# Kernel optimization log

Measured on AMD Instinct MI355X. Metric: run time of the kernel, lower is better.

Reference implementation:

```python
import jax, jax.numpy as jnp
import numpy as np
from math import log, sqrt

B, S, D, H, L = 16, 512, 512, 8, 6
DPH = D // H
DFF = 2048
VOCAB = 1024
MAXDEG = 64
NPC, NS = 4096, 4096


def setup_inputs() -> dict:
    rng = np.random.default_rng(0)
    raw_x = rng.integers(0, VOCAB + 1, (B, S)).astype(np.int32)
    scatter_degree = rng.integers(0, MAXDEG + 1, (B, S)).astype(np.int32)

    def uniq_triples(n, seed):
        r = np.random.default_rng(seed)
        flat = r.choice(B * S * S, n, replace=False)  # unique (b,i,j)
        b, i, j = np.unravel_index(flat, (B, S, S))
        return np.stack([b, i, j], 1).astype(np.int32)

    parentchild_indices = uniq_triples(NPC, 1)
    silbing_indices = uniq_triples(NS, 2)
    parent_child_now = np.stack([np.arange(B), rng.integers(0, S, B)], 1).astype(np.int32)
    silbing_now = np.stack([np.arange(B), rng.integers(0, S, B)], 1).astype(np.int32)

    key = jax.random.key(0)
    ks = jax.random.split(key, 16)
    sc = 0.02
    inp = {
        "raw_x": jnp.asarray(raw_x),
        "scatter_degree": jnp.asarray(scatter_degree),
        "parentchild_indices": jnp.asarray(parentchild_indices),
        "parent_child_now": jnp.asarray(parent_child_now),
        "silbing_indices": jnp.asarray(silbing_indices),
        "silbing_now": jnp.asarray(silbing_now),
        "vocab_emb": jax.random.normal(ks[0], (VOCAB + 1, D), jnp.float32) * sc,
        "degree_emb": jax.random.normal(ks[1], (MAXDEG + 1, D), jnp.float32) * sc,
        "active_rel_emb": jax.random.normal(ks[2], (2, D), jnp.float32) * sc,
        "relation_encoder": jax.random.uniform(ks[3], (3,), jnp.float32),
        "Wq": jax.random.normal(ks[4], (L, D, D), jnp.float32) * sc,
        "bq": jnp.zeros((L, D), jnp.float32),
        "Wk": jax.random.normal(ks[5], (L, D, D), jnp.float32) * sc,
        "bk": jnp.zeros((L, D), jnp.float32),
        "Wv": jax.random.normal(ks[6], (L, D, D), jnp.float32) * sc,
        "bv": jnp.zeros((L, D), jnp.float32),
        "Wo": jax.random.normal(ks[7], (L, D, D), jnp.float32) * sc,
        "bo": jnp.zeros((L, D), jnp.float32),
        "W1": jax.random.normal(ks[8], (L, DFF, D), jnp.float32) * sc,
        "b1": jnp.zeros((L, DFF), jnp.float32),
        "W2": jax.random.normal(ks[9], (L, D, DFF), jnp.float32) * sc,
        "b2": jnp.zeros((L, D), jnp.float32),
        "ln_g": jnp.ones((L, D), jnp.float32),
        "ln_b": jnp.zeros((L, D), jnp.float32),
        "logits_w": jax.random.normal(ks[10], (VOCAB, D), jnp.float32) * sc,
    }
    return inp


def _layer_norm(x, g, b):
    m = jnp.mean(x, -1, keepdims=True)
    v = jnp.mean((x - m) ** 2, -1, keepdims=True)  # biased var, eps=1e-5 (torch default)
    return (x - m) * jax.lax.rsqrt(v + 1e-5) * g + b


def _forward(raw_x, scatter_degree, parentchild_indices, parent_child_now,
             silbing_indices, silbing_now, vocab_emb, degree_emb, active_rel_emb,
             relation_encoder, Wq, bq, Wk, bk, Wv, bv, Wo, bo, W1, b1, W2, b2,
             ln_g, ln_b, logits_w):
    x = vocab_emb[raw_x]  # [B,S,D]
    # sinusoidal positional encoding
    pos = jnp.arange(S, dtype=jnp.float32)[:, None]
    div = jnp.exp(jnp.arange(0, D, 2, dtype=jnp.float32) * (-log(10000.0) / D))
    pe = jnp.zeros((S, D), x.dtype).at[:, 0::2].set(jnp.sin(pos * div)).at[:, 1::2].set(jnp.cos(pos * div))
    x = x + pe
    # structural encodings
    x = x + degree_emb[scatter_degree]
    x = x.at[parent_child_now[:, 0], parent_child_now[:, 1]].add(active_rel_emb[0])
    x = x.at[silbing_now[:, 0], silbing_now[:, 1]].add(active_rel_emb[1])

    pb, pi, pj = parentchild_indices[:, 0], parentchild_indices[:, 1], parentchild_indices[:, 2]
    sb, si, sj = silbing_indices[:, 0], silbing_indices[:, 1], silbing_indices[:, 2]
    inv_norm = 1.0 / sqrt(DPH)

    for l in range(L):
        q = (x @ Wq[l].T + bq[l]).reshape(B, S, H, DPH).transpose(0, 2, 1, 3)
        k = (x @ Wk[l].T + bk[l]).reshape(B, S, H, DPH).transpose(0, 2, 1, 3)
        v = (x @ Wv[l].T + bv[l]).reshape(B, S, H, DPH).transpose(0, 2, 1, 3)
        scores = jnp.einsum('bhqd,bhkd->bhqk', q, k) * inv_norm  # [B,H,S,S]
        # scatter-added relational bias (broadcast over all heads)
        scores = scores.at[pb, :, pi, pj].add(relation_encoder[0])
        scores = scores.at[pb, :, pj, pi].add(relation_encoder[1])
        scores = scores.at[sb, :, si, sj].add(relation_encoder[2])
        scores = scores.at[sb, :, sj, si].add(relation_encoder[2])
        attn = jax.nn.softmax(scores, axis=-1)
        o = jnp.einsum('bhqk,bhkd->bhqd', attn, v).transpose(0, 2, 1, 3).reshape(B, S, D)
        o = o @ Wo[l].T + bo[l]
        x = _layer_norm(x + o, ln_g[l], ln_b[l])
        ff = jax.nn.relu(x @ W1[l].T + b1[l]) @ W2[l].T + b2[l]
        x = _layer_norm(x + ff, ln_g[l], ln_b[l])

    return x[:, -1] @ logits_w.T  # [B, VOCAB]


def reference(raw_x, scatter_degree, parentchild_indices, parent_child_now,
              silbing_indices, silbing_now, vocab_emb, degree_emb, active_rel_emb,
              relation_encoder, Wq, bq, Wk, bk, Wv, bv, Wo, bo, W1, b1, W2, b2,
              ln_g, ln_b, logits_w):
    return _forward(raw_x, scatter_degree, parentchild_indices, parent_child_now,
                    silbing_indices, silbing_now, vocab_emb, degree_emb, active_rel_emb,
                    relation_encoder, Wq, bq, Wk, bk, Wv, bv, Wo, bo, W1, b1, W2, b2,
                    ln_g, ln_b, logits_w)
```

## Files before the change

kernel.cpp:

```cpp
#include <hip/hip_runtime.h>
#include <hip/hip_bf16.h>
#include <math.h>

#define B_ 16
#define S_ 512
#define D_ 512
#define H_ 8
#define L_ 6
#define DPH_ 64
#define DFF_ 2048
#define VOCAB_ 1024
#define NPC_ 4096
#define NS_ 4096
#define BS_ (B_ * S_)
#define LOG2E 1.4426950408889634f

typedef __attribute__((ext_vector_type(8))) short bf16x8;
typedef __attribute__((ext_vector_type(4))) float f32x4;

__device__ __forceinline__ ushort f2bf(float f) {
    __hip_bfloat16 h = __float2bfloat16(f);
    return __builtin_bit_cast(ushort, h);
}
__device__ __forceinline__ float bf2f(ushort u) {
    unsigned int v = ((unsigned int)u) << 16;
    return __builtin_bit_cast(float, v);
}

__global__ __launch_bounds__(256) void embed_kernel(
    const int* __restrict__ raw_x, const int* __restrict__ sdeg,
    const float* __restrict__ vemb, const float* __restrict__ demb,
    float* __restrict__ x)
{
    size_t idx = (size_t)blockIdx.x * 256 + threadIdx.x;
    int d = (int)(idx & (D_ - 1));
    size_t bs = idx >> 9;
    int s = (int)(bs & (S_ - 1));
    int tok = raw_x[bs];
    int dg  = sdeg[bs];
    float e = expf(-(float)(d & ~1) * (9.210340371976184f / (float)D_));
    float ang = (float)s * e;
    float pe = (d & 1) ? cosf(ang) : sinf(ang);
    x[idx] = vemb[(size_t)tok * D_ + d] + pe + demb[(size_t)dg * D_ + d];
}

__global__ void relnow_kernel(const int* __restrict__ pcn, const int* __restrict__ sbn,
                              const float* __restrict__ arel, float* __restrict__ x)
{
    int b = blockIdx.x;
    int t = threadIdx.x;
    int b1 = pcn[b * 2 + 0], p1 = pcn[b * 2 + 1];
    x[((size_t)(b1 * S_ + p1)) * D_ + t] += arel[t];
    int b2 = sbn[b * 2 + 0], p2 = sbn[b * 2 + 1];
    x[((size_t)(b2 * S_ + p2)) * D_ + t] += arel[D_ + t];
}

__global__ void bias_scatter_kernel(const int* __restrict__ pc, const int* __restrict__ sb,
                                    const float* __restrict__ renc, float* __restrict__ bias)
{
    int t = blockIdx.x * 256 + threadIdx.x;
    float r0 = renc[0], r1 = renc[1], r2 = renc[2];
    if (t < NPC_) {
        int b = pc[t * 3 + 0], i = pc[t * 3 + 1], j = pc[t * 3 + 2];
        atomicAdd(&bias[((size_t)b * S_ + i) * S_ + j], r0);
        atomicAdd(&bias[((size_t)b * S_ + j) * S_ + i], r1);
    } else if (t < NPC_ + NS_) {
        int u = t - NPC_;
        int b = sb[u * 3 + 0], i = sb[u * 3 + 1], j = sb[u * 3 + 2];
        atomicAdd(&bias[((size_t)b * S_ + i) * S_ + j], r2);
        atomicAdd(&bias[((size_t)b * S_ + j) * S_ + i], r2);
    }
}

__global__ __launch_bounds__(256) void bias_cast_kernel(const float* __restrict__ src,
                                                        ushort* __restrict__ dst)
{
    int i = blockIdx.x * 256 + threadIdx.x;
    float4 v = ((const float4*)src)[i];
    ushort4 o;
    o.x = f2bf(v.x * LOG2E); o.y = f2bf(v.y * LOG2E);
    o.z = f2bf(v.z * LOG2E); o.w = f2bf(v.w * LOG2E);
    ((ushort4*)dst)[i] = o;
}

__global__ __launch_bounds__(256) void cast4_kernel(const float* __restrict__ src,
                                                    ushort* __restrict__ dst, int n4)
{
    int i = blockIdx.x * 256 + threadIdx.x;
    if (i >= n4) return;
    float4 v = ((const float4*)src)[i];
    ushort4 o;
    o.x = f2bf(v.x); o.y = f2bf(v.y); o.z = f2bf(v.z); o.w = f2bf(v.w);
    ((ushort4*)dst)[i] = o;
}

__global__ __launch_bounds__(256) void pack_qkv_kernel(
    const float* __restrict__ Wq, const float* __restrict__ Wk, const float* __restrict__ Wv,
    ushort* __restrict__ dst)
{
    int idx = blockIdx.x * 256 + threadIdx.x;
    int c = idx & 511;
    int rl = idx >> 9;
    int r = rl % 1536, l = rl / 1536;
    float v;
    if (r < 512)       v = Wq[((size_t)l * 512 + r) * 512 + c];
    else if (r < 1024) v = Wk[((size_t)l * 512 + (r - 512)) * 512 + c];
    else               v = Wv[((size_t)l * 512 + (r - 1024)) * 512 + c];
    dst[idx] = f2bf(v);
}

__global__ void pack_bqkv_kernel(const float* __restrict__ bq, const float* __restrict__ bk,
                                 const float* __restrict__ bv, float* __restrict__ dst)
{
    int idx = blockIdx.x * 256 + threadIdx.x;
    if (idx >= L_ * 1536) return;
    int r = idx % 1536, l = idx / 1536;
    float v;
    if (r < 512)       v = bq[l * 512 + r];
    else if (r < 1024) v = bk[l * 512 + r - 512];
    else               v = bv[l * 512 + r - 1024];
    dst[idx] = v;
}

#define GL2LDS(g, l) __builtin_amdgcn_global_load_lds( \
    (const __attribute__((address_space(1))) void*)(g), \
    (__attribute__((address_space(3))) void*)(l), 16, 0, 0)

__global__ __launch_bounds__(256) void gemm_bf16(
    const ushort* __restrict__ A, const ushort* __restrict__ W,
    const float* __restrict__ bias, ushort* __restrict__ Cb,
    int K, int M, int mode)
{
    __shared__ ushort As0[128 * 32];
    __shared__ ushort As1[128 * 32];
    __shared__ ushort Bs0[128 * 32];
    __shared__ ushort Bs1[128 * 32];

    const int t  = threadIdx.x;
    const int wv = t >> 6;
    const int ln = t & 63;
    const int wm = wv >> 1, wn = wv & 1;
    const int lq = ln >> 4, lc = ln & 15;
    const int row0 = blockIdx.x * 128;
    const int col0 = blockIdx.y * 128;
    const int lr = ln >> 2;
    const int lk = (ln & 3) * 8;

    f32x4 acc[4][4] = {};

    for (int k0 = 0; k0 < K; k0 += 64) {
        #pragma unroll
        for (int i = 0; i < 2; i++) {
            int r = i * 64 + wv * 16;
            const ushort* ga = A + (size_t)(row0 + r + lr) * K + k0 + lk;
            const ushort* gb = W + (size_t)(col0 + r + lr) * K + k0 + lk;
            GL2LDS(ga,      &As0[r * 32]);
            GL2LDS(gb,      &Bs0[r * 32]);
            GL2LDS(ga + 32, &As1[r * 32]);
            GL2LDS(gb + 32, &Bs1[r * 32]);
        }
        __syncthreads();

        bf16x8 af[4], bf[4];
        #pragma unroll
        for (int mi = 0; mi < 4; mi++)
            af[mi] = *(const bf16x8*)&As0[(wm * 64 + mi * 16 + lc) * 32 + lq * 8];
        #pragma unroll
        for (int ni = 0; ni < 4; ni++)
            bf[ni] = *(const bf16x8*)&Bs0[(wn * 64 + ni * 16 + lc) * 32 + lq * 8];
        #pragma unroll
        for (int mi = 0; mi < 4; mi++)
            #pragma unroll
            for (int ni = 0; ni < 4; ni++)
                acc[mi][ni] = __builtin_amdgcn_mfma_f32_16x16x32_bf16(af[mi], bf[ni], acc[mi][ni], 0, 0, 0);

        #pragma unroll
        for (int mi = 0; mi < 4; mi++)
            af[mi] = *(const bf16x8*)&As1[(wm * 64 + mi * 16 + lc) * 32 + lq * 8];
        #pragma unroll
        for (int ni = 0; ni < 4; ni++)
            bf[ni] = *(const bf16x8*)&Bs1[(wn * 64 + ni * 16 + lc) * 32 + lq * 8];
        #pragma unroll
        for (int mi = 0; mi < 4; mi++)
            #pragma unroll
            for (int ni = 0; ni < 4; ni++)
                acc[mi][ni] = __builtin_amdgcn_mfma_f32_16x16x32_bf16(af[mi], bf[ni], acc[mi][ni], 0, 0, 0);
        __syncthreads();
    }

    #pragma unroll
    for (int mi = 0; mi < 4; mi++) {
        #pragma unroll
        for (int ni = 0; ni < 4; ni++) {
            int gcol = col0 + wn * 64 + ni * 16 + lc;
            float bb = bias[gcol];
            #pragma unroll
            for (int rr = 0; rr < 4; rr++) {
                int grow = row0 + wm * 64 + mi * 16 + lq * 4 + rr;
                float val = acc[mi][ni][rr] + bb;
                if (mode == 1) val = fmaxf(val, 0.f);
                Cb[(size_t)grow * M + gcol] = f2bf(val);
            }
        }
    }
}

__global__ __launch_bounds__(256) void gemm64(
    const ushort* __restrict__ A, const ushort* __restrict__ W,
    float* __restrict__ C, int K, int M)
{
    __shared__ ushort As0[128 * 32];
    __shared__ ushort As1[128 * 32];
    __shared__ ushort Bs0[64 * 32];
    __shared__ ushort Bs1[64 * 32];

    const int t  = threadIdx.x;
    const int wv = t >> 6;
    const int ln = t & 63;
    const int wm = wv >> 1, wn = wv & 1;
    const int lq = ln >> 4, lc = ln & 15;
    const int row0 = blockIdx.x * 128;
    const int col0 = blockIdx.y * 64;
    const int lr = ln >> 2;
    const int lk = (ln & 3) * 8;

    f32x4 acc[4][2] = {};

    for (int k0 = 0; k0 < K; k0 += 64) {
        #pragma unroll
        for (int i = 0; i < 2; i++) {
            int r = i * 64 + wv * 16;
            const ushort* ga = A + (size_t)(row0 + r + lr) * K + k0 + lk;
            GL2LDS(ga,      &As0[r * 32]);
            GL2LDS(ga + 32, &As1[r * 32]);
        }
        {
            int rb = wv * 16;
            const ushort* gb = W + (size_t)(col0 + rb + lr) * K + k0 + lk;
            GL2LDS(gb,      &Bs0[rb * 32]);
            GL2LDS(gb + 32, &Bs1[rb * 32]);
        }
        __syncthreads();

        bf16x8 af[4], bf[2];
        #pragma unroll
        for (int mi = 0; mi < 4; mi++)
            af[mi] = *(const bf16x8*)&As0[(wm * 64 + mi * 16 + lc) * 32 + lq * 8];
        #pragma unroll
        for (int ni = 0; ni < 2; ni++)
            bf[ni] = *(const bf16x8*)&Bs0[(wn * 32 + ni * 16 + lc) * 32 + lq * 8];
        #pragma unroll
        for (int mi = 0; mi < 4; mi++)
            #pragma unroll
            for (int ni = 0; ni < 2; ni++)
                acc[mi][ni] = __builtin_amdgcn_mfma_f32_16x16x32_bf16(af[mi], bf[ni], acc[mi][ni], 0, 0, 0);

        #pragma unroll
        for (int mi = 0; mi < 4; mi++)
            af[mi] = *(const bf16x8*)&As1[(wm * 64 + mi * 16 + lc) * 32 + lq * 8];
        #pragma unroll
        for (int ni = 0; ni < 2; ni++)
            bf[ni] = *(const bf16x8*)&Bs1[(wn * 32 + ni * 16 + lc) * 32 + lq * 8];
        #pragma unroll
        for (int mi = 0; mi < 4; mi++)
            #pragma unroll
            for (int ni = 0; ni < 2; ni++)
                acc[mi][ni] = __builtin_amdgcn_mfma_f32_16x16x32_bf16(af[mi], bf[ni], acc[mi][ni], 0, 0, 0);
        __syncthreads();
    }

    #pragma unroll
    for (int mi = 0; mi < 4; mi++)
        #pragma unroll
        for (int ni = 0; ni < 2; ni++) {
            int gcol = col0 + wn * 32 + ni * 16 + lc;
            #pragma unroll
            for (int rr = 0; rr < 4; rr++) {
                int grow = row0 + wm * 64 + mi * 16 + lq * 4 + rr;
                C[(size_t)grow * M + gcol] = acc[mi][ni][rr];
            }
        }
}

#define PSTR 72

__device__ __forceinline__ int vswz(int d, int j) {
    int g = ((j >> 3) ^ (d & 7) ^ ((d >> 3) & 7)) & 7;
    return d * 64 + g * 8 + (j & 7);
}

__global__ __launch_bounds__(256) void attn_kernel(
    const ushort* __restrict__ qkv, const ushort* __restrict__ biasb,
    ushort* __restrict__ ao)
{
    const int qt = blockIdx.x, h = blockIdx.y, b = blockIdx.z;
    const int t  = threadIdx.x;
    const int wq = t >> 6;
    const int ln = t & 63;
    const int lq = ln >> 4;
    const int lc = ln & 15;
    const int r  = t >> 2;
    const int cg = t & 3;

    __shared__ ushort Qs[64 * PSTR];
    __shared__ ushort Ks[64 * PSTR];
    __shared__ ushort Ps[64 * PSTR];
    __shared__ ushort Vts[64 * 64];

    const int i0 = qt * 64;

    {
        const ushort* qsrc = qkv + (size_t)(b * S_ + i0 + r) * 1536 + h * 64 + cg * 16;
        *(uint4*)&Qs[r * PSTR + cg * 16]     = ((const uint4*)qsrc)[0];
        *(uint4*)&Qs[r * PSTR + cg * 16 + 8] = ((const uint4*)qsrc)[1];
    }
    bf16x8 aq0 = *(const bf16x8*)&Qs[(wq * 16 + lc) * PSTR + lq * 8];
    bf16x8 aq1 = *(const bf16x8*)&Qs[(wq * 16 + lc) * PSTR + 32 + lq * 8];

    f32x4 of[4] = {};
    float l_lane[4] = {};
    const float QSC = 0.125f * LOG2E;

    for (int j0 = 0; j0 < S_; j0 += 64) {
        __syncthreads();
        {
            const ushort* ksrc = qkv + (size_t)(b * S_ + j0 + r) * 1536 + 512 + h * 64 + cg * 16;
            *(uint4*)&Ks[r * PSTR + cg * 16]     = ((const uint4*)ksrc)[0];
            *(uint4*)&Ks[r * PSTR + cg * 16 + 8] = ((const uint4*)ksrc)[1];
            const ushort* vsrc = ksrc + 512;
            ushort vv[16];
            *(uint4*)&vv[0] = ((const uint4*)vsrc)[0];
            *(uint4*)&vv[8] = ((const uint4*)vsrc)[1];
            #pragma unroll
            for (int dd = 0; dd < 16; dd++)
                Vts[vswz(cg * 16 + dd, r)] = vv[dd];
        }
        __syncthreads();

        f32x4 sf[4] = {};
        #pragma unroll
        for (int ni = 0; ni < 4; ni++) {
            bf16x8 bk0 = *(const bf16x8*)&Ks[(ni * 16 + lc) * PSTR + lq * 8];
            bf16x8 bk1 = *(const bf16x8*)&Ks[(ni * 16 + lc) * PSTR + 32 + lq * 8];
            sf[ni] = __builtin_amdgcn_mfma_f32_16x16x32_bf16(aq0, bk0, sf[ni], 0, 0, 0);
            sf[ni] = __builtin_amdgcn_mfma_f32_16x16x32_bf16(aq1, bk1, sf[ni], 0, 0, 0);
        }

        const ushort* bbase = biasb + (size_t)(b * S_ + i0 + wq * 16 + lq * 4) * S_ + j0;
        #pragma unroll
        for (int ni = 0; ni < 4; ni++)
            #pragma unroll
            for (int rr = 0; rr < 4; rr++) {
                float bv = bf2f(bbase[(size_t)rr * S_ + ni * 16 + lc]);
                float p = __builtin_amdgcn_exp2f(fmaf(sf[ni][rr], QSC, bv));
                l_lane[rr] += p;
                Ps[(wq * 16 + lq * 4 + rr) * PSTR + ni * 16 + lc] = f2bf(p);
            }

        bf16x8 ap0 = *(const bf16x8*)&Ps[(wq * 16 + lc) * PSTR + lq * 8];
        bf16x8 ap1 = *(const bf16x8*)&Ps[(wq * 16 + lc) * PSTR + 32 + lq * 8];
        #pragma unroll
        for (int ni = 0; ni < 4; ni++) {
            bf16x8 bv0 = *(const bf16x8*)&Vts[vswz(ni * 16 + lc, lq * 8)];
            bf16x8 bv1 = *(const bf16x8*)&Vts[vswz(ni * 16 + lc, 32 + lq * 8)];
            of[ni] = __builtin_amdgcn_mfma_f32_16x16x32_bf16(ap0, bv0, of[ni], 0, 0, 0);
            of[ni] = __builtin_amdgcn_mfma_f32_16x16x32_bf16(ap1, bv1, of[ni], 0, 0, 0);
        }
    }

    float inv[4];
    #pragma unroll
    for (int rr = 0; rr < 4; rr++) {
        float s = l_lane[rr];
        s += __shfl_xor(s, 1);
        s += __shfl_xor(s, 2);
        s += __shfl_xor(s, 4);
        s += __shfl_xor(s, 8);
        inv[rr] = 1.f / s;
    }
    #pragma unroll
    for (int ni = 0; ni < 4; ni++)
        #pragma unroll
        for (int rr = 0; rr < 4; rr++) {
            int row = i0 + wq * 16 + lq * 4 + rr;
            ao[(size_t)(b * S_ + row) * D_ + h * 64 + ni * 16 + lc] = f2bf(of[ni][rr] * inv[rr]);
        }
}

__device__ __forceinline__ float block_sum(float v, float* red) {
    #pragma unroll
    for (int off = 32; off > 0; off >>= 1) v += __shfl_down(v, off);
    int t = threadIdx.x;
    if ((t & 63) == 0) red[t >> 6] = v;
    __syncthreads();
    float r = red[0] + red[1] + red[2] + red[3];
    __syncthreads();
    return r;
}

__global__ __launch_bounds__(256) void add_ln_kernel(
    float* __restrict__ x, const float* __restrict__ p,
    const float* __restrict__ bvec,
    const float* __restrict__ g, const float* __restrict__ bta,
    ushort* __restrict__ xb)
{
    __shared__ float red[4];
    const int row = blockIdx.x;
    const int t = threadIdx.x;
    const size_t base = (size_t)row * D_;
    float v0 = x[base + t]       + p[base + t]       + bvec[t];
    float v1 = x[base + t + 256] + p[base + t + 256] + bvec[t + 256];
    float mean = block_sum(v0 + v1, red) * (1.f / (float)D_);
    float d0 = v0 - mean, d1 = v1 - mean;
    float var = block_sum(d0 * d0 + d1 * d1, red) * (1.f / (float)D_);
    float inv = rsqrtf(var + 1e-5f);
    float o0 = d0 * inv * g[t] + bta[t];
    float o1 = d1 * inv * g[t + 256] + bta[t + 256];
    x[base + t] = o0;
    x[base + t + 256] = o1;
    xb[base + t] = f2bf(o0);
    xb[base + t + 256] = f2bf(o1);
}

__global__ __launch_bounds__(256) void logits_kernel(
    const float* __restrict__ x, const float* __restrict__ lw, float* __restrict__ out)
{
    __shared__ float xs[D_];
    const int b = blockIdx.x;
    const int vchunk = blockIdx.y;
    const int t = threadIdx.x;
    const float* xrow = x + ((size_t)(b * S_ + (S_ - 1)) * D_);
    xs[t] = xrow[t];
    xs[t + 256] = xrow[t + 256];
    __syncthreads();
    for (int vv = vchunk * 128 + t; vv < vchunk * 128 + 128; vv += 256) {
        const float* wr = lw + (size_t)vv * D_;
        float acc = 0.f;
        #pragma unroll 8
        for (int d = 0; d < D_; d += 4) {
            float4 w4 = *(const float4*)&wr[d];
            acc += xs[d] * w4.x + xs[d + 1] * w4.y + xs[d + 2] * w4.z + xs[d + 3] * w4.w;
        }
        out[(size_t)b * VOCAB_ + vv] = acc;
    }
}

extern "C" void kernel_launch(void* const* d_in, const int* in_sizes, int n_in,
                              void* d_out, int out_size, void* d_ws, size_t ws_size,
                              hipStream_t stream)
{
    const int* raw_x = (const int*)d_in[0];
    const int* sdeg  = (const int*)d_in[1];
    const int* pci   = (const int*)d_in[2];
    const int* pcn   = (const int*)d_in[3];
    const int* sbi   = (const int*)d_in[4];
    const int* sbn   = (const int*)d_in[5];
    const float* vemb = (const float*)d_in[6];
    const float* demb = (const float*)d_in[7];
    const float* arel = (const float*)d_in[8];
    const float* renc = (const float*)d_in[9];
    const float* Wq = (const float*)d_in[10];
    const float* bq = (const float*)d_in[11];
    const float* Wk = (const float*)d_in[12];
    const float* bk = (const float*)d_in[13];
    const float* Wv = (const float*)d_in[14];
    const float* bv = (const float*)d_in[15];
    const float* Wo = (const float*)d_in[16];
    const float* bo = (const float*)d_in[17];
    const float* W1 = (const float*)d_in[18];
    const float* b1 = (const float*)d_in[19];
    const float* W2 = (const float*)d_in[20];
    const float* b2 = (const float*)d_in[21];
    const float* lng = (const float*)d_in[22];
    const float* lnb = (const float*)d_in[23];
    const float* lw  = (const float*)d_in[24];
    float* out = (float*)d_out;

    float* wsf = (float*)d_ws;
    const size_t X = (size_t)BS_ * D_;
    float*  x    = wsf;
    ushort* xb   = (ushort*)(wsf + X);
    ushort* qkvb = (ushort*)(wsf + (X * 3) / 2);
    ushort* ao   = (ushort*)(wsf + 3 * X);
    ushort* h1   = (ushort*)(wsf + (X * 7) / 2);
    float*  proj = wsf + (X * 11) / 2;
    float*  bias = wsf + (X * 13) / 2;
    ushort* biasb= (ushort*)(wsf + (X * 15) / 2);
    ushort* wb   = (ushort*)(wsf + 8 * X);
    ushort* wqkv_b = wb;
    ushort* wo_b   = wb + 4718592;
    ushort* w1_b   = wb + 6291456;
    ushort* w2_b   = wb + 12582912;
    float*  bqkv   = wsf + 8 * X + 9437184;

    embed_kernel<<<(B_ * S_ * D_) / 256, 256, 0, stream>>>(raw_x, sdeg, vemb, demb, x);
    relnow_kernel<<<B_, D_, 0, stream>>>(pcn, sbn, arel, x);
    cast4_kernel<<<(int)(X / 4 / 256), 256, 0, stream>>>(x, xb, (int)(X / 4));

    hipMemsetAsync(bias, 0, (size_t)B_ * S_ * S_ * sizeof(float), stream);
    bias_scatter_kernel<<<(NPC_ + NS_ + 255) / 256, 256, 0, stream>>>(pci, sbi, renc, bias);
    bias_cast_kernel<<<(B_ * S_ * S_ / 4) / 256, 256, 0, stream>>>(bias, biasb);

    pack_qkv_kernel<<<(L_ * 1536 * 512) / 256, 256, 0, stream>>>(Wq, Wk, Wv, wqkv_b);
    pack_bqkv_kernel<<<(L_ * 1536 + 255) / 256, 256, 0, stream>>>(bq, bk, bv, bqkv);
    cast4_kernel<<<(L_ * 512 * 512) / 4 / 256, 256, 0, stream>>>(Wo, wo_b, L_ * 512 * 512 / 4);
    cast4_kernel<<<(L_ * 2048 * 512) / 4 / 256, 256, 0, stream>>>(W1, w1_b, L_ * 2048 * 512 / 4);
    cast4_kernel<<<(L_ * 512 * 2048) / 4 / 256, 256, 0, stream>>>(W2, w2_b, L_ * 512 * 2048 / 4);

    dim3 blk(256);
    for (int l = 0; l < L_; l++) {
        gemm_bf16<<<dim3(BS_ / 128, 1536 / 128), blk, 0, stream>>>(
            xb, wqkv_b + (size_t)l * 1536 * 512, bqkv + l * 1536, qkvb, 512, 1536, 2);

        attn_kernel<<<dim3(S_ / 64, H_, B_), blk, 0, stream>>>(qkvb, biasb, ao);

        gemm64<<<dim3(BS_ / 128, 512 / 64), blk, 0, stream>>>(
            ao, wo_b + (size_t)l * 512 * 512, proj, 512, 512);
        add_ln_kernel<<<BS_, blk, 0, stream>>>(x, proj, bo + l * 512,
                                               lng + l * D_, lnb + l * D_, xb);

        gemm_bf16<<<dim3(BS_ / 128, 2048 / 128), blk, 0, stream>>>(
            xb, w1_b + (size_t)l * 2048 * 512, b1 + l * 2048, h1, 512, 2048, 1);
        gemm64<<<dim3(BS_ / 128, 512 / 64), blk, 0, stream>>>(
            h1, w2_b + (size_t)l * 512 * 2048, proj, 2048, 512);
        add_ln_kernel<<<BS_, blk, 0, stream>>>(x, proj, b2 + l * 512,
                                               lng + l * D_, lnb + l * D_, xb);
    }

    logits_kernel<<<dim3(B_, 8), blk, 0, stream>>>(x, lw, out);
}
```

Measured before the change: 1.156 ms.

## Keep residual stream and projection outputs in bf16, dropping fp32 copies

Removes the fp32 residual buffer and makes the embedding, residual, projection GEMM outputs and layernorm all read and write bf16 only. The separate cast kernel after embedding disappears, and the add+layernorm kernels move half as many bytes for x and the projection. The cost is precision: the residual stream is rounded to bf16 at every layer, so error can accumulate over the six layers.

```diff
diff --git a/kernel.cpp b/kernel.cpp
--- a/kernel.cpp
+++ b/kernel.cpp
@@ -30,7 +30,7 @@
 __global__ __launch_bounds__(256) void embed_kernel(
     const int* __restrict__ raw_x, const int* __restrict__ sdeg,
     const float* __restrict__ vemb, const float* __restrict__ demb,
-    float* __restrict__ x)
+    ushort* __restrict__ xb)
 {
     size_t idx = (size_t)blockIdx.x * 256 + threadIdx.x;
     int d = (int)(idx & (D_ - 1));
@@ -41,18 +41,20 @@
     float e = expf(-(float)(d & ~1) * (9.210340371976184f / (float)D_));
     float ang = (float)s * e;
     float pe = (d & 1) ? cosf(ang) : sinf(ang);
-    x[idx] = vemb[(size_t)tok * D_ + d] + pe + demb[(size_t)dg * D_ + d];
+    xb[idx] = f2bf(vemb[(size_t)tok * D_ + d] + pe + demb[(size_t)dg * D_ + d]);
 }
 
 __global__ void relnow_kernel(const int* __restrict__ pcn, const int* __restrict__ sbn,
-                              const float* __restrict__ arel, float* __restrict__ x)
+                              const float* __restrict__ arel, ushort* __restrict__ xb)
 {
     int b = blockIdx.x;
     int t = threadIdx.x;
     int b1 = pcn[b * 2 + 0], p1 = pcn[b * 2 + 1];
-    x[((size_t)(b1 * S_ + p1)) * D_ + t] += arel[t];
+    size_t i1 = ((size_t)(b1 * S_ + p1)) * D_ + t;
+    xb[i1] = f2bf(bf2f(xb[i1]) + arel[t]);
     int b2 = sbn[b * 2 + 0], p2 = sbn[b * 2 + 1];
-    x[((size_t)(b2 * S_ + p2)) * D_ + t] += arel[D_ + t];
+    size_t i2 = ((size_t)(b2 * S_ + p2)) * D_ + t;
+    xb[i2] = f2bf(bf2f(xb[i2]) + arel[D_ + t]);
 }
 
 __global__ void bias_scatter_kernel(const int* __restrict__ pc, const int* __restrict__ sb,
@@ -207,7 +209,7 @@
 
 __global__ __launch_bounds__(256) void gemm64(
     const ushort* __restrict__ A, const ushort* __restrict__ W,
-    float* __restrict__ C, int K, int M)
+    ushort* __restrict__ Cb, int K, int M)
 {
     __shared__ ushort As0[128 * 32];
     __shared__ ushort As1[128 * 32];
@@ -277,7 +279,7 @@
             #pragma unroll
             for (int rr = 0; rr < 4; rr++) {
                 int grow = row0 + wm * 64 + mi * 16 + lq * 4 + rr;
-                C[(size_t)grow * M + gcol] = acc[mi][ni][rr];
+                Cb[(size_t)grow * M + gcol] = f2bf(acc[mi][ni][rr]);
             }
         }
 }
@@ -399,39 +401,36 @@
 }
 
 __global__ __launch_bounds__(256) void add_ln_kernel(
-    float* __restrict__ x, const float* __restrict__ p,
+    ushort* __restrict__ xb, const ushort* __restrict__ pb,
     const float* __restrict__ bvec,
-    const float* __restrict__ g, const float* __restrict__ bta,
-    ushort* __restrict__ xb)
+    const float* __restrict__ g, const float* __restrict__ bta)
 {
     __shared__ float red[4];
     const int row = blockIdx.x;
     const int t = threadIdx.x;
     const size_t base = (size_t)row * D_;
-    float v0 = x[base + t]       + p[base + t]       + bvec[t];
-    float v1 = x[base + t + 256] + p[base + t + 256] + bvec[t + 256];
+    float v0 = bf2f(xb[base + t])       + bf2f(pb[base + t])       + bvec[t];
+    float v1 = bf2f(xb[base + t + 256]) + bf2f(pb[base + t + 256]) + bvec[t + 256];
     float mean = block_sum(v0 + v1, red) * (1.f / (float)D_);
     float d0 = v0 - mean, d1 = v1 - mean;
     float var = block_sum(d0 * d0 + d1 * d1, red) * (1.f / (float)D_);
     float inv = rsqrtf(var + 1e-5f);
     float o0 = d0 * inv * g[t] + bta[t];
     float o1 = d1 * inv * g[t + 256] + bta[t + 256];
-    x[base + t] = o0;
-    x[base + t + 256] = o1;
-    xb[base + t] = f2bf(o0);
+    xb[base + t]       = f2bf(o0);
     xb[base + t + 256] = f2bf(o1);
 }
 
 __global__ __launch_bounds__(256) void logits_kernel(
-    const float* __restrict__ x, const float* __restrict__ lw, float* __restrict__ out)
+    const ushort* __restrict__ xb, const float* __restrict__ lw, float* __restrict__ out)
 {
     __shared__ float xs[D_];
     const int b = blockIdx.x;
     const int vchunk = blockIdx.y;
     const int t = threadIdx.x;
-    const float* xrow = x + ((size_t)(b * S_ + (S_ - 1)) * D_);
-    xs[t] = xrow[t];
-    xs[t + 256] = xrow[t + 256];
+    const ushort* xrow = xb + ((size_t)(b * S_ + (S_ - 1)) * D_);
+    xs[t] = bf2f(xrow[t]);
+    xs[t + 256] = bf2f(xrow[t + 256]);
     __syncthreads();
     for (int vv = vchunk * 128 + t; vv < vchunk * 128 + 128; vv += 256) {
         const float* wr = lw + (size_t)vv * D_;
@@ -478,24 +477,22 @@
 
     float* wsf = (float*)d_ws;
     const size_t X = (size_t)BS_ * D_;
-    float*  x    = wsf;
-    ushort* xb   = (ushort*)(wsf + X);
-    ushort* qkvb = (ushort*)(wsf + (X * 3) / 2);
-    ushort* ao   = (ushort*)(wsf + 3 * X);
-    ushort* h1   = (ushort*)(wsf + (X * 7) / 2);
-    float*  proj = wsf + (X * 11) / 2;
-    float*  bias = wsf + (X * 13) / 2;
-    ushort* biasb= (ushort*)(wsf + (X * 15) / 2);
-    ushort* wb   = (ushort*)(wsf + 8 * X);
+    ushort* xb   = (ushort*)wsf;
+    ushort* qkvb = (ushort*)(wsf + X / 2);
+    ushort* ao   = (ushort*)(wsf + 2 * X);
+    ushort* h1   = (ushort*)(wsf + (X * 5) / 2);
+    ushort* projb= (ushort*)(wsf + (X * 9) / 2);
+    float*  bias = wsf + 5 * X;
+    ushort* biasb= (ushort*)(wsf + 6 * X);
+    ushort* wb   = (ushort*)(wsf + (X * 13) / 2);
     ushort* wqkv_b = wb;
     ushort* wo_b   = wb + 4718592;
     ushort* w1_b   = wb + 6291456;
     ushort* w2_b   = wb + 12582912;
-    float*  bqkv   = wsf + 8 * X + 9437184;
-
-    embed_kernel<<<(B_ * S_ * D_) / 256, 256, 0, stream>>>(raw_x, sdeg, vemb, demb, x);
-    relnow_kernel<<<B_, D_, 0, stream>>>(pcn, sbn, arel, x);
-    cast4_kernel<<<(int)(X / 4 / 256), 256, 0, stream>>>(x, xb, (int)(X / 4));
+    float*  bqkv   = wsf + (X * 13) / 2 + 9437184;
+
+    embed_kernel<<<(B_ * S_ * D_) / 256, 256, 0, stream>>>(raw_x, sdeg, vemb, demb, xb);
+    relnow_kernel<<<B_, D_, 0, stream>>>(pcn, sbn, arel, xb);
 
     hipMemsetAsync(bias, 0, (size_t)B_ * S_ * S_ * sizeof(float), stream);
     bias_scatter_kernel<<<(NPC_ + NS_ + 255) / 256, 256, 0, stream>>>(pci, sbi, renc, bias);
@@ -515,17 +512,17 @@
         attn_kernel<<<dim3(S_ / 64, H_, B_), blk, 0, stream>>>(qkvb, biasb, ao);
 
         gemm64<<<dim3(BS_ / 128, 512 / 64), blk, 0, stream>>>(
-            ao, wo_b + (size_t)l * 512 * 512, proj, 512, 512);
-        add_ln_kernel<<<BS_, blk, 0, stream>>>(x, proj, bo + l * 512,
-                                               lng + l * D_, lnb + l * D_, xb);
+            ao, wo_b + (size_t)l * 512 * 512, projb, 512, 512);
+        add_ln_kernel<<<BS_, blk, 0, stream>>>(xb, projb, bo + l * 512,
+                                               lng + l * D_, lnb + l * D_);
 
         gemm_bf16<<<dim3(BS_ / 128, 2048 / 128), blk, 0, stream>>>(
             xb, w1_b + (size_t)l * 2048 * 512, b1 + l * 2048, h1, 512, 2048, 1);
         gemm64<<<dim3(BS_ / 128, 512 / 64), blk, 0, stream>>>(
-            h1, w2_b + (size_t)l * 512 * 2048, proj, 2048, 512);
-        add_ln_kernel<<<BS_, blk, 0, stream>>>(x, proj, b2 + l * 512,
-                                               lng + l * D_, lnb + l * D_, xb);
-    }
-
-    logits_kernel<<<dim3(B_, 8), blk, 0, stream>>>(x, lw, out);
-}
+            h1, w2_b + (size_t)l * 512 * 2048, projb, 2048, 512);
+        add_ln_kernel<<<BS_, blk, 0, stream>>>(xb, projb, b2 + l * 512,
+                                               lng + l * D_, lnb + l * D_);
+    }
+
+    logits_kernel<<<dim3(B_, 8), blk, 0, stream>>>(xb, lw, out);
+}
```

Result: faster. 1.082 ms (-6.4%).
